# Performance work log

Measured on AMD Instinct MI355X. Metric: run time of the kernel, lower is better.

The kernel has to match this reference:

```python
import jax, jax.numpy as jnp
import numpy as np

B, C, H, W = 2, 64, 96, 96
DQK = C // 8  # query/key channel dim = 8


def setup_inputs() -> dict:
    key = jax.random.key(0)
    ks = jax.random.split(key, 8)
    s = 0.05
    x = jax.random.normal(ks[0], (B, C, H, W), dtype=jnp.float32)
    Wq = jax.random.normal(ks[1], (DQK, C), dtype=jnp.float32) * s
    bq = jax.random.normal(ks[2], (DQK,), dtype=jnp.float32) * s
    Wk = jax.random.normal(ks[3], (DQK, C), dtype=jnp.float32) * s
    bk = jax.random.normal(ks[4], (DQK,), dtype=jnp.float32) * s
    Wv = jax.random.normal(ks[5], (C, C), dtype=jnp.float32) * s
    bv = jax.random.normal(ks[6], (C,), dtype=jnp.float32) * s
    gamma = jax.random.normal(ks[7], (1,), dtype=jnp.float32) * s
    return {"x": x, "Wq": Wq, "bq": bq, "Wk": Wk, "bk": bk,
            "Wv": Wv, "bv": bv, "gamma": gamma}


def _attend(x, Wq, bq, Wk, bk, Wv, bv, gamma):
    b, c, h, w = x.shape
    p = h * w
    xf = x.reshape(b, c, p)                                    # [B,C,P]
    # 1x1 convs == per-pixel linear maps
    q = jnp.einsum('dc,bcp->bpd', Wq, xf) + bq                 # [B,P,d]
    k = jnp.einsum('dc,bcp->bdp', Wk, xf) + bk[None, :, None]  # [B,d,P]
    v = jnp.einsum('oc,bcp->bop', Wv, xf) + bv[None, :, None]  # [B,C,P]
    # energy[b,i,j] = q_i . k_j ; softmax over keys j (no 1/sqrt(d) scale,
    # matching the original module)
    energy = jnp.einsum('bpd,bdq->bpq', q, k)                  # [B,P,P]
    attn = jax.nn.softmax(energy, axis=-1)                     # [B,P,P]
    out = jnp.einsum('bcq,bpq->bcp', v, attn)                  # [B,C,P]
    out = out.reshape(b, c, h, w)
    return gamma * out + x


def reference(x, Wq, bq, Wk, bk, Wv, bv, gamma):
    return _attend(x, Wq, bq, Wk, bk, Wv, bv, gamma)
```

## Files before the change

kernel.cpp:

```cpp
#include <hip/hip_runtime.h>
#include <hip/hip_bf16.h>
#include <stdint.h>

#define BB 2
#define CC 64
#define PP 9216
#define QTILES 144
#define LOG2E 1.4426950408889634f
#define SCH_C 16248.664965f

typedef unsigned short ushort;
typedef __attribute__((ext_vector_type(8))) short short8;
typedef __attribute__((ext_vector_type(4))) float floatx4;
typedef __attribute__((ext_vector_type(4))) int intx4;

__device__ __forceinline__ ushort f2bf(float f) {
    unsigned int u = __float_as_uint(f);
    u = (u + 0x7fffu + ((u >> 16) & 1u)) >> 16;
    return (ushort)u;
}

__device__ __forceinline__ unsigned int exp2_pk_bf16(float e0, float e1) {
    const int i0 = (int)fmaf(e0, 128.f, SCH_C);
    const int i1 = (int)fmaf(e1, 128.f, SCH_C);
    return (unsigned int)i0 | ((unsigned int)i1 << 16);
}

__global__ __launch_bounds__(256)
void proj3(const float* __restrict__ x,
           const float* __restrict__ Wq, const float* __restrict__ bq,
           const float* __restrict__ Wk, const float* __restrict__ bk,
           const float* __restrict__ Wv, const float* __restrict__ bv,
           ushort* __restrict__ qbuf, ushort* __restrict__ kbuf,
           ushort* __restrict__ vfw)
{
    const int tid = threadIdx.x;
    const int px  = tid & 63;
    const int og  = __builtin_amdgcn_readfirstlane(tid >> 6);
    const int blk = blockIdx.x;
    const int b     = blk / (2 * QTILES);
    const int rem   = blk % (2 * QTILES);
    const int ptile = rem >> 1;
    const int rhalf = rem & 1;
    const int p     = ptile * 64 + px;
    const int r0    = rhalf * 40 + og * 10;

    const float* wr[10];
#pragma unroll
    for (int r = 0; r < 10; ++r) {
        const int row = r0 + r;
        wr[r] = (row < 8) ? (Wq + row * 64)
              : (row < 16) ? (Wk + (row - 8) * 64)
              : (Wv + (row - 16) * 64);
    }

    float xv[64];
#pragma unroll
    for (int c = 0; c < 64; ++c)
        xv[c] = x[((size_t)b * 64 + c) * PP + p];

    float acc[10];
#pragma unroll
    for (int r = 0; r < 10; ++r) acc[r] = 0.f;
#pragma unroll
    for (int c = 0; c < 64; ++c) {
#pragma unroll
        for (int r = 0; r < 10; ++r)
            acc[r] = fmaf(wr[r][c], xv[c], acc[r]);
    }

#pragma unroll
    for (int r = 0; r < 10; ++r) {
        const int row = r0 + r;
        if (row < 8) {
            const float v = (acc[r] + bq[row]) * LOG2E;
            qbuf[((size_t)b * PP + p) * 8 + row] = f2bf(v);
        } else if (row < 16) {
            const float v = acc[r] + bk[row - 8];
            kbuf[((size_t)b * PP + p) * 8 + (row - 8)] = f2bf(v);
        } else {
            const int co = row - 16;
            const float v = acc[r] + bv[co];
            const int pl = p & 31;
            const int ps = (p & ~31) | ((((pl >> 2) & 3) << 3) | (((pl >> 4) & 1) << 2) | (pl & 3));
            vfw[((size_t)b * 64 + co) * PP + ps] = f2bf(v);
        }
    }
}

__global__ __launch_bounds__(128, 3)
void attn7(const ushort* __restrict__ qbuf, const ushort* __restrict__ kbuf,
           const ushort* __restrict__ vfw,
           ushort* __restrict__ accp, float* __restrict__ lsump,
           int keysPerG, int numTiles)
{
    __shared__ __align__(16) float smerge[64 * 64];
    __shared__ float slsum[64];

    const int tid  = threadIdx.x;
    const int lane = tid & 63;
    const int wid  = tid >> 6;
    const int col  = lane & 15;
    const int quad = lane >> 4;

    const int qt = blockIdx.x % QTILES;
    const int gb = blockIdx.x / QTILES;
    const int b  = gb % BB;
    const int g  = gb / BB;
    const int q0 = qt * 64;

    const short8 zf = {0, 0, 0, 0, 0, 0, 0, 0};
    const short vone = (short)0x3F80;
    const short8 vones = {vone, vone, vone, vone, vone, vone, vone, vone};

    short8 qfragB[4];
#pragma unroll
    for (int qh = 0; qh < 4; ++qh)
        qfragB[qh] = (quad == 0)
            ? *(const short8*)(qbuf + ((size_t)b * PP + q0 + qh * 16 + col) * 8)
            : zf;

    floatx4 acc[4][4];
#pragma unroll
    for (int qh = 0; qh < 4; ++qh)
#pragma unroll
        for (int cb = 0; cb < 4; ++cb) acc[qh][cb] = (floatx4){0.f, 0.f, 0.f, 0.f};
    floatx4 accLh[4];
#pragma unroll
    for (int qh = 0; qh < 4; ++qh) accLh[qh] = (floatx4){0.f, 0.f, 0.f, 0.f};

    const ushort* kB = kbuf + (size_t)b * PP * 8;
    const ushort* vB = vfw + (size_t)b * 64 * PP;
    const int kwbase = g * keysPerG + wid * 32;

    short8 kf0c = *(const short8*)(kB + (size_t)(kwbase + col) * 8 + quad * 8);
    short8 kf1c = *(const short8*)(kB + (size_t)(kwbase + 16 + col) * 8 + quad * 8);
    short8 vfc[4];
#pragma unroll
    for (int cb = 0; cb < 4; ++cb)
        vfc[cb] = *(const short8*)(vB + ((size_t)(cb * 16 + col)) * PP + kwbase + quad * 8);

    for (int t = 0; t < numTiles; ++t) {
        const int tn  = (t + 1 < numTiles) ? (t + 1) : t;
        const int kwn = kwbase + tn * 64;

        const short8 kf0n = *(const short8*)(kB + (size_t)(kwn + col) * 8 + quad * 8);
        const short8 kf1n = *(const short8*)(kB + (size_t)(kwn + 16 + col) * 8 + quad * 8);
        short8 vfn[4];
#pragma unroll
        for (int cb = 0; cb < 4; ++cb)
            vfn[cb] = *(const short8*)(vB + ((size_t)(cb * 16 + col)) * PP + kwn + quad * 8);

#pragma unroll
        for (int qh = 0; qh < 4; ++qh) {
            const floatx4 E0 = __builtin_amdgcn_mfma_f32_16x16x32_bf16(
                kf0c, qfragB[qh], (floatx4){0.f, 0.f, 0.f, 0.f}, 0, 0, 0);
            const floatx4 E1 = __builtin_amdgcn_mfma_f32_16x16x32_bf16(
                kf1c, qfragB[qh], (floatx4){0.f, 0.f, 0.f, 0.f}, 0, 0, 0);

            intx4 pi;
            pi.x = (int)exp2_pk_bf16(E0[0], E0[1]);
            pi.y = (int)exp2_pk_bf16(E0[2], E0[3]);
            pi.z = (int)exp2_pk_bf16(E1[0], E1[1]);
            pi.w = (int)exp2_pk_bf16(E1[2], E1[3]);
            const short8 pf = __builtin_bit_cast(short8, pi);

            accLh[qh] = __builtin_amdgcn_mfma_f32_16x16x32_bf16(vones, pf, accLh[qh], 0, 0, 0);
#pragma unroll
            for (int cb = 0; cb < 4; ++cb)
                acc[qh][cb] = __builtin_amdgcn_mfma_f32_16x16x32_bf16(
                    vfc[cb], pf, acc[qh][cb], 0, 0, 0);
        }

        kf0c = kf0n;
        kf1c = kf1n;
#pragma unroll
        for (int cb = 0; cb < 4; ++cb) vfc[cb] = vfn[cb];
    }

    if (wid == 1) {
#pragma unroll
        for (int qh = 0; qh < 4; ++qh)
#pragma unroll
            for (int cb = 0; cb < 4; ++cb)
#pragma unroll
                for (int r = 0; r < 4; ++r)
                    smerge[(cb * 16 + quad * 4 + r) * 64 + qh * 16 + col] = acc[qh][cb][r];
        if (quad == 0)
#pragma unroll
            for (int qh = 0; qh < 4; ++qh)
                slsum[qh * 16 + col] = accLh[qh][0];
    }
    __syncthreads();
    if (wid == 0) {
        ushort* ab = accp + ((size_t)g * BB + b) * CC * PP;
#pragma unroll
        for (int qh = 0; qh < 4; ++qh)
#pragma unroll
            for (int cb = 0; cb < 4; ++cb)
#pragma unroll
                for (int r = 0; r < 4; ++r) {
                    const int c = cb * 16 + quad * 4 + r;
                    const float v = acc[qh][cb][r] + smerge[c * 64 + qh * 16 + col];
                    ab[(size_t)c * PP + q0 + qh * 16 + col] = f2bf(v);
                }
        if (quad == 0) {
            float* lb = lsump + ((size_t)g * BB + b) * PP + q0;
#pragma unroll
            for (int qh = 0; qh < 4; ++qh)
                lb[qh * 16 + col] = accLh[qh][0] + slsum[qh * 16 + col];
        }
    }
}

__global__ __launch_bounds__(256)
void combine(const ushort* __restrict__ accp, const float* __restrict__ lsump,
             const float* __restrict__ x, const float* __restrict__ gamma,
             float* __restrict__ out, int G)
{
    const size_t i8 = ((size_t)blockIdx.x * 256 + threadIdx.x) * 8;
    const int b = (int)(i8 / ((size_t)CC * PP));
    const int p = (int)(i8 % PP);
    const float gm = gamma[0];

    float asum[8] = {}, lst[8] = {};
    for (int g = 0; g < G; ++g) {
        const uint4 av = *(const uint4*)(accp + (size_t)g * (BB * CC * PP) + i8);
        const unsigned int u[4] = {av.x, av.y, av.z, av.w};
#pragma unroll
        for (int k = 0; k < 4; ++k) {
            asum[2 * k]     += __uint_as_float(u[k] << 16);
            asum[2 * k + 1] += __uint_as_float(u[k] & 0xffff0000u);
        }
        const float* lp = lsump + ((size_t)g * BB + b) * PP + p;
        const float4 l0 = *(const float4*)lp;
        const float4 l1 = *(const float4*)(lp + 4);
        lst[0] += l0.x; lst[1] += l0.y; lst[2] += l0.z; lst[3] += l0.w;
        lst[4] += l1.x; lst[5] += l1.y; lst[6] += l1.z; lst[7] += l1.w;
    }

    const float4 x0 = *(const float4*)(x + i8);
    const float4 x1 = *(const float4*)(x + i8 + 4);
    float o[8] = {x0.x, x0.y, x0.z, x0.w, x1.x, x1.y, x1.z, x1.w};
#pragma unroll
    for (int j = 0; j < 8; ++j)
        o[j] = fmaf(asum[j], gm / fmaxf(lst[j], 1e-30f), o[j]);
    *(float4*)(out + i8)     = make_float4(o[0], o[1], o[2], o[3]);
    *(float4*)(out + i8 + 4) = make_float4(o[4], o[5], o[6], o[7]);
}

extern "C" void kernel_launch(void* const* d_in, const int* in_sizes, int n_in,
                              void* d_out, int out_size, void* d_ws, size_t ws_size,
                              hipStream_t stream)
{
    const float* x     = (const float*)d_in[0];
    const float* Wq    = (const float*)d_in[1];
    const float* bq    = (const float*)d_in[2];
    const float* Wk    = (const float*)d_in[3];
    const float* bk    = (const float*)d_in[4];
    const float* Wv    = (const float*)d_in[5];
    const float* bv    = (const float*)d_in[6];
    const float* gamma = (const float*)d_in[7];
    float* out = (float*)d_out;

    const size_t nQK  = (size_t)BB * PP * 8;
    const size_t nV   = (size_t)BB * CC * PP;
    const size_t base = 2 * nQK * 2 + nV * 2;
    const size_t perG = nV * 2 + (size_t)BB * PP * 4;
    const int G = (ws_size >= base + 8 * perG) ? 8
                : (ws_size >= base + 6 * perG) ? 6
                : (ws_size >= base + 4 * perG) ? 4 : 2;
    const int keysPerG = PP / G;
    const int numTiles = keysPerG / 64;

    ushort* qbuf = (ushort*)d_ws;
    ushort* kbuf = qbuf + nQK;
    ushort* vfw  = kbuf + nQK;
    ushort* accp = vfw + nV;
    float* lsump = (float*)(accp + (size_t)G * nV);

    proj3<<<dim3(BB * 2 * QTILES), dim3(256), 0, stream>>>(
        x, Wq, bq, Wk, bk, Wv, bv, qbuf, kbuf, vfw);
    attn7<<<dim3(G * BB * QTILES), dim3(128), 0, stream>>>(
        qbuf, kbuf, vfw, accp, lsump, keysPerG, numTiles);
    combine<<<dim3(576), dim3(256), 0, stream>>>(
        accp, lsump, x, gamma, out, G);
}
```

Baseline: 138.6 us.

## Double-buffer key/value tiles, cheaper packed exp2, and cap key splits at four

The attention loop now ping-pongs between two register sets of K/V fragments and unrolls by two, which removes the register copies at the end of each iteration and gives loads more time to land. The Schraudolph exp2 now adds a large bias constant in float and packs the two bf16 halves with a byte-permute instead of two float-to-int conversions plus shift/or. The key-split count G is capped at 4 instead of up to 8, which halves the partial-buffer traffic in combine but lowers grid parallelism. The unroll-by-two assumes numTiles is even; with G=4 it is 36, and with G=2 it is 72.

```diff
diff --git a/kernel.cpp b/kernel.cpp
--- a/kernel.cpp
+++ b/kernel.cpp
@@ -8,6 +8,7 @@
 #define QTILES 144
 #define LOG2E 1.4426950408889634f
 #define SCH_C 16248.664965f
+#define SCH_BC 12599160.0f
 
 typedef unsigned short ushort;
 typedef __attribute__((ext_vector_type(8))) short short8;
@@ -21,9 +22,10 @@
 }
 
 __device__ __forceinline__ unsigned int exp2_pk_bf16(float e0, float e1) {
-    const int i0 = (int)fmaf(e0, 128.f, SCH_C);
-    const int i1 = (int)fmaf(e1, 128.f, SCH_C);
-    return (unsigned int)i0 | ((unsigned int)i1 << 16);
+    const float t0 = fmaf(e0, 128.f, SCH_BC);
+    const float t1 = fmaf(e1, 128.f, SCH_BC);
+    return __builtin_amdgcn_perm(__float_as_uint(t1), __float_as_uint(t0),
+                                 0x05040100u);
 }
 
 __global__ __launch_bounds__(256)
@@ -89,7 +91,7 @@
 }
 
 __global__ __launch_bounds__(128, 3)
-void attn7(const ushort* __restrict__ qbuf, const ushort* __restrict__ kbuf,
+void attn8(const ushort* __restrict__ qbuf, const ushort* __restrict__ kbuf,
            const ushort* __restrict__ vfw,
            ushort* __restrict__ accp, float* __restrict__ lsump,
            int keysPerG, int numTiles)
@@ -133,30 +135,23 @@
     const ushort* vB = vfw + (size_t)b * 64 * PP;
     const int kwbase = g * keysPerG + wid * 32;
 
-    short8 kf0c = *(const short8*)(kB + (size_t)(kwbase + col) * 8 + quad * 8);
-    short8 kf1c = *(const short8*)(kB + (size_t)(kwbase + 16 + col) * 8 + quad * 8);
-    short8 vfc[4];
-#pragma unroll
-    for (int cb = 0; cb < 4; ++cb)
-        vfc[cb] = *(const short8*)(vB + ((size_t)(cb * 16 + col)) * PP + kwbase + quad * 8);
-
-    for (int t = 0; t < numTiles; ++t) {
-        const int tn  = (t + 1 < numTiles) ? (t + 1) : t;
-        const int kwn = kwbase + tn * 64;
-
-        const short8 kf0n = *(const short8*)(kB + (size_t)(kwn + col) * 8 + quad * 8);
-        const short8 kf1n = *(const short8*)(kB + (size_t)(kwn + 16 + col) * 8 + quad * 8);
-        short8 vfn[4];
+    auto tile_load = [&](int t, short8& kf0, short8& kf1, short8 (&vf)[4]) {
+        const int kw = kwbase + t * 64;
+        kf0 = *(const short8*)(kB + (size_t)(kw + col) * 8 + quad * 8);
+        kf1 = *(const short8*)(kB + (size_t)(kw + 16 + col) * 8 + quad * 8);
 #pragma unroll
         for (int cb = 0; cb < 4; ++cb)
-            vfn[cb] = *(const short8*)(vB + ((size_t)(cb * 16 + col)) * PP + kwn + quad * 8);
-
+            vf[cb] = *(const short8*)(vB + ((size_t)(cb * 16 + col)) * PP + kw + quad * 8);
+    };
+
+    auto tile_compute = [&](const short8& kf0, const short8& kf1,
+                            const short8 (&vf)[4]) {
 #pragma unroll
         for (int qh = 0; qh < 4; ++qh) {
             const floatx4 E0 = __builtin_amdgcn_mfma_f32_16x16x32_bf16(
-                kf0c, qfragB[qh], (floatx4){0.f, 0.f, 0.f, 0.f}, 0, 0, 0);
+                kf0, qfragB[qh], (floatx4){0.f, 0.f, 0.f, 0.f}, 0, 0, 0);
             const floatx4 E1 = __builtin_amdgcn_mfma_f32_16x16x32_bf16(
-                kf1c, qfragB[qh], (floatx4){0.f, 0.f, 0.f, 0.f}, 0, 0, 0);
+                kf1, qfragB[qh], (floatx4){0.f, 0.f, 0.f, 0.f}, 0, 0, 0);
 
             intx4 pi;
             pi.x = (int)exp2_pk_bf16(E0[0], E0[1]);
@@ -169,13 +164,20 @@
 #pragma unroll
             for (int cb = 0; cb < 4; ++cb)
                 acc[qh][cb] = __builtin_amdgcn_mfma_f32_16x16x32_bf16(
-                    vfc[cb], pf, acc[qh][cb], 0, 0, 0);
-        }
-
-        kf0c = kf0n;
-        kf1c = kf1n;
-#pragma unroll
-        for (int cb = 0; cb < 4; ++cb) vfc[cb] = vfn[cb];
+                    vf[cb], pf, acc[qh][cb], 0, 0, 0);
+        }
+    };
+
+    short8 kf0A, kf1A, vfA[4];
+    short8 kf0B, kf1B, vfB[4];
+    tile_load(0, kf0A, kf1A, vfA);
+
+    for (int t = 0; t < numTiles; t += 2) {
+        tile_load(t + 1, kf0B, kf1B, vfB);
+        tile_compute(kf0A, kf1A, vfA);
+        const int t2 = (t + 2 < numTiles) ? (t + 2) : (t + 1);
+        tile_load(t2, kf0A, kf1A, vfA);
+        tile_compute(kf0B, kf1B, vfB);
     }
 
     if (wid == 1) {
@@ -267,9 +269,7 @@
     const size_t nV   = (size_t)BB * CC * PP;
     const size_t base = 2 * nQK * 2 + nV * 2;
     const size_t perG = nV * 2 + (size_t)BB * PP * 4;
-    const int G = (ws_size >= base + 8 * perG) ? 8
-                : (ws_size >= base + 6 * perG) ? 6
-                : (ws_size >= base + 4 * perG) ? 4 : 2;
+    const int G = (ws_size >= base + 4 * perG) ? 4 : 2;
     const int keysPerG = PP / G;
     const int numTiles = keysPerG / 64;
 
@@ -281,7 +281,7 @@
 
     proj3<<<dim3(BB * 2 * QTILES), dim3(256), 0, stream>>>(
         x, Wq, bq, Wk, bk, Wv, bv, qbuf, kbuf, vfw);
-    attn7<<<dim3(G * BB * QTILES), dim3(128), 0, stream>>>(
+    attn8<<<dim3(G * BB * QTILES), dim3(128), 0, stream>>>(
         qbuf, kbuf, vfw, accp, lsump, keysPerG, numTiles);
     combine<<<dim3(576), dim3(256), 0, stream>>>(
         accp, lsump, x, gamma, out, G);
```

After: 140.1 us. Within noise of the previous version (+1.1%).
